# Kernel tuning notes

Measured on AMD Instinct MI355X. Metric: run time of the kernel, lower is better.

## Reference

```python
import jax, jax.numpy as jnp
import numpy as np

D_MODEL = 1024
N_HEADS = 16
HEAD_DIM = D_MODEL // N_HEADS
D_FF = 4096
LN_EPS = 1e-5


def setup_inputs() -> dict:
    key = jax.random.key(0)
    ks = jax.random.split(key, 13)
    s = lambda fan_in: 1.0 / np.sqrt(fan_in)
    return {
        "x": jax.random.normal(ks[0], (2, 2048, D_MODEL), dtype=jnp.float32),
        "w_qkv": jax.random.uniform(ks[1], (D_MODEL, 3 * D_MODEL), jnp.float32, -s(D_MODEL), s(D_MODEL)),
        "b_qkv": jax.random.uniform(ks[2], (3 * D_MODEL,), jnp.float32, -s(D_MODEL), s(D_MODEL)),
        "w_out": jax.random.uniform(ks[3], (D_MODEL, D_MODEL), jnp.float32, -s(D_MODEL), s(D_MODEL)),
        "b_out": jax.random.uniform(ks[4], (D_MODEL,), jnp.float32, -s(D_MODEL), s(D_MODEL)),
        "w_ff1": jax.random.uniform(ks[5], (D_MODEL, D_FF), jnp.float32, -s(D_MODEL), s(D_MODEL)),
        "b_ff1": jax.random.uniform(ks[6], (D_FF,), jnp.float32, -s(D_MODEL), s(D_MODEL)),
        "w_ff2": jax.random.uniform(ks[7], (D_FF, D_MODEL), jnp.float32, -s(D_FF), s(D_FF)),
        "b_ff2": jax.random.uniform(ks[8], (D_MODEL,), jnp.float32, -s(D_FF), s(D_FF)),
        "ln1_g": jnp.ones((D_MODEL,), jnp.float32),
        "ln1_b": jnp.zeros((D_MODEL,), jnp.float32),
        "ln2_g": jnp.ones((D_MODEL,), jnp.float32),
        "ln2_b": jnp.zeros((D_MODEL,), jnp.float32),
    }


def _layer_norm(x, g, b):
    mu = jnp.mean(x, axis=-1, keepdims=True)
    var = jnp.mean(jnp.square(x - mu), axis=-1, keepdims=True)
    return (x - mu) * jax.lax.rsqrt(var + LN_EPS) * g + b


def reference(x, w_qkv, b_qkv, w_out, b_out, w_ff1, b_ff1, w_ff2, b_ff2,
              ln1_g, ln1_b, ln2_g, ln2_b):
    B, S, D = x.shape
    scale = HEAD_DIM ** -0.5
    qkv = x @ w_qkv + b_qkv                                   # [B,S,3D]
    qkv = qkv.reshape(B, S, 3, N_HEADS, HEAD_DIM)
    q, k, v = (qkv[:, :, 0], qkv[:, :, 1], qkv[:, :, 2])      # [B,S,H,Dh]
    attn = jnp.einsum("bqhd,bkhd->bhqk", q, k) * scale        # [B,H,S,S]
    attn = jax.nn.softmax(attn, axis=-1)
    o = jnp.einsum("bhqk,bkhd->bqhd", attn, v).reshape(B, S, D)
    o = o @ w_out + b_out
    x = _layer_norm(x + o, ln1_g, ln1_b)
    # FFN: Linear -> exact GELU -> Linear (dropout = 0)
    h = jax.nn.gelu(x @ w_ff1 + b_ff1, approximate=False)
    ff = h @ w_ff2 + b_ff2
    x = _layer_norm(x + ff, ln2_g, ln2_b)
    return x
```

## Files before the change

kernel.cpp:

```cpp
#include <hip/hip_runtime.h>
#include <hip/hip_bf16.h>
#include <cstdint>
#include <cstddef>

using bf16 = __hip_bfloat16;
typedef __attribute__((ext_vector_type(8))) short bf16x8;
typedef __attribute__((ext_vector_type(4))) float f32x4;

#define TOKENS 4096
#define DMODEL 1024
#define DFF    4096
#define SEQ    2048
#define NHEAD  16
#define HDIM   64
#define KVBLK  64
#define NT     (SEQ / KVBLK)
#define QSCALE 0.1803368801111f

__device__ __forceinline__ void async16(const void* g, void* l) {
  __builtin_amdgcn_global_load_lds(
      (const __attribute__((address_space(1))) void*)g,
      (__attribute__((address_space(3))) void*)l, 16, 0, 0);
}

__device__ __forceinline__ f32x4 mfma16(bf16x8 a, bf16x8 b, f32x4 c) {
  return __builtin_amdgcn_mfma_f32_16x16x32_bf16(a, b, c, 0, 0, 0);
}

__device__ __forceinline__ float exp2_fast(float x) {
  float r;
  asm("v_exp_f32 %0, %1" : "=v"(r) : "v"(x));
  return r;
}

__device__ __forceinline__ float gelu_fast(float x) {
  const float z = fabsf(x) * 0.70710678118f;
  const float t = __builtin_amdgcn_rcpf(1.f + 0.3275911f * z);
  float p = 1.061405429f;
  p = p * t - 1.453152027f;
  p = p * t + 1.421413741f;
  p = p * t - 0.284496736f;
  p = p * t + 0.254829592f;
  const float e = exp2_fast(-z * z * 1.44269504089f);
  float erf = 1.f - p * t * e;
  erf = (x < 0.f) ? -erf : erf;
  return 0.5f * x * (1.f + erf);
}

__global__ void cast_bf16_k(const float* __restrict__ src, bf16* __restrict__ dst, int n) {
  int i = (blockIdx.x * blockDim.x + threadIdx.x) * 4;
  if (i >= n) return;
  float4 v = *(const float4*)(src + i);
  dst[i + 0] = __float2bfloat16(v.x);
  dst[i + 1] = __float2bfloat16(v.y);
  dst[i + 2] = __float2bfloat16(v.z);
  dst[i + 3] = __float2bfloat16(v.w);
}

__global__ void transpose_cast_k(const float* __restrict__ src, bf16* __restrict__ dst,
                                 int K, int N) {
  __shared__ float tile[32][33];
  int nt = blockIdx.x * 32, kt = blockIdx.y * 32;
  int tx = threadIdx.x, ty = threadIdx.y;
  #pragma unroll
  for (int i = 0; i < 32; i += 8)
    tile[ty + i][tx] = src[(size_t)(kt + ty + i) * N + nt + tx];
  __syncthreads();
  #pragma unroll
  for (int i = 0; i < 32; i += 8)
    dst[(size_t)(nt + ty + i) * K + kt + tx] = __float2bfloat16(tile[tx][ty + i]);
}

template <int EPI, int BN>
__global__ __launch_bounds__(256, 2)
void gemm_bt(const bf16* __restrict__ A, const bf16* __restrict__ Bt,
             const float* __restrict__ bias, int M, int N, int K,
             float* __restrict__ outf, float* __restrict__ outf2,
             bf16* __restrict__ outb,
             bf16* __restrict__ Qb, bf16* __restrict__ Kb, bf16* __restrict__ Vtb) {
  constexpr int MR = (BN == 128) ? 4 : 2;
  __shared__ bf16 Al[2][128 * 32];
  __shared__ bf16 Bl[2][BN * 32];
  const int t = threadIdx.x;
  const int nwg = gridDim.x * gridDim.y;
  const int flat = blockIdx.y * gridDim.x + blockIdx.x;
  const int swz = (flat & 7) * (nwg >> 3) + (flat >> 3);
  const int bm = (swz / gridDim.x) * 128, bn = (swz % gridDim.x) * BN;
  const int kz = blockIdx.z;
  const int Ksub = K / gridDim.z;
  const int kb0 = kz * Ksub;
  const int wid = t >> 6, lane = t & 63, g = lane >> 4, r = lane & 15;
  const int wr = (BN == 128) ? (wid >> 1) * 64 : wid * 32;
  const int wc = (BN == 128) ? (wid & 1) * 64 : 0;

  const f32x4 zero = {0.f, 0.f, 0.f, 0.f};
  f32x4 acc[MR][4];
  #pragma unroll
  for (int i = 0; i < MR; i++)
    #pragma unroll
    for (int j = 0; j < 4; j++) acc[i][j] = zero;

  const int ar0 = t >> 2, ac = (t & 3) * 8;
  const int ar1 = ar0 + 64;
  const int ach0 = t * 16, ach1 = ach0 + 4096;

  const int NK = Ksub >> 5;
  #define STAGE(ktile, pb)                                                          \
    do {                                                                            \
      const int kk = kb0 + ((ktile) << 5);                                          \
      async16(A + (size_t)(bm + ar0) * K + kk + ac, (char*)Al[pb] + ach0);          \
      async16(A + (size_t)(bm + ar1) * K + kk + ac, (char*)Al[pb] + ach1);          \
      async16(Bt + (size_t)(bn + ar0) * K + kk + ac, (char*)Bl[pb] + ach0);         \
      if constexpr (BN == 128)                                                      \
        async16(Bt + (size_t)(bn + ar1) * K + kk + ac, (char*)Bl[pb] + ach1);       \
    } while (0)

  STAGE(0, 0);
  asm volatile("s_waitcnt vmcnt(0)" ::: "memory");
  __builtin_amdgcn_s_barrier();

  #pragma unroll 1
  for (int it = 0; it < NK; ++it) {
    const int cur = it & 1;
    if (it + 1 < NK) STAGE(it + 1, cur ^ 1);
    bf16x8 af[MR], bfr[4];
    #pragma unroll
    for (int mt = 0; mt < MR; mt++)
      af[mt] = *(const bf16x8*)&Al[cur][(wr + mt * 16 + r) * 32 + 8 * g];
    #pragma unroll
    for (int nt = 0; nt < 4; nt++)
      bfr[nt] = *(const bf16x8*)&Bl[cur][(wc + nt * 16 + r) * 32 + 8 * g];
    #pragma unroll
    for (int mt = 0; mt < MR; mt++)
      #pragma unroll
      for (int nt = 0; nt < 4; nt++)
        acc[mt][nt] = mfma16(af[mt], bfr[nt], acc[mt][nt]);
    __builtin_amdgcn_sched_barrier(0);
    asm volatile("s_waitcnt vmcnt(0)" ::: "memory");
    __builtin_amdgcn_s_barrier();
  }
  #undef STAGE

  float* __restrict__ pdst = kz ? outf2 : outf;
  #pragma unroll
  for (int nt = 0; nt < 4; nt++) {
    const int col = bn + wc + nt * 16 + r;
    const float bv = (EPI == 3) ? 0.f : bias[col];
    #pragma unroll
    for (int mt = 0; mt < MR; mt++) {
      #pragma unroll
      for (int j = 0; j < 4; j++) {
        const int row = bm + wr + mt * 16 + 4 * g + j;
        float v = acc[mt][nt][j] + bv;
        if constexpr (EPI == 0) {
          const int part = col >> 10, hd = col & 1023, h = hd >> 6, d = hd & 63;
          const int b_ = row >> 11, s_ = row & 2047;
          if (part == 0) {
            Qb[((size_t)(b_ * NHEAD + h) * SEQ + s_) * HDIM + d] =
                __float2bfloat16(v * QSCALE);
          } else if (part == 1) {
            Kb[((size_t)(b_ * NHEAD + h) * SEQ + s_) * HDIM + d] = __float2bfloat16(v);
          } else {
            Vtb[((size_t)(b_ * NHEAD + h) * HDIM + d) * SEQ + s_] = __float2bfloat16(v);
          }
        } else if constexpr (EPI == 3) {
          pdst[(size_t)row * N + col] = v;
        } else {
          outb[(size_t)row * N + col] = __float2bfloat16(gelu_fast(v));
        }
      }
    }
  }
}

__global__ __launch_bounds__(256, 4)
void attn_k(const bf16* __restrict__ Q, const bf16* __restrict__ Km,
            const bf16* __restrict__ Vt, bf16* __restrict__ O) {
  __shared__ bf16 Kl[2][KVBLK * 64];
  __shared__ bf16 Vl[2][KVBLK * 64];
  __shared__ bf16 P[4][16 * 64];
  const int b = blockIdx.x;
  const int bswz = (b & 7) * 128 + (b >> 3);
  const int bh = bswz >> 5, qb = bswz & 31;
  const int t = threadIdx.x, wid = t >> 6, lane = t & 63, g = lane >> 4, r = lane & 15;
  const int q0 = qb * 64 + wid * 16;
  const bf16* Qp = Q + (size_t)bh * SEQ * HDIM;
  const char* Kc = (const char*)(Km + (size_t)bh * SEQ * HDIM);
  const char* Vc = (const char*)(Vt + (size_t)bh * HDIM * SEQ);

  const bf16x8 qf0 = *(const bf16x8*)&Qp[(q0 + r) * HDIM + 8 * g];
  const bf16x8 qf1 = *(const bf16x8*)&Qp[(q0 + r) * HDIM + 8 * g + 32];

  const int o0 = wid * 2048 + lane * 16, o1 = o0 + 1024;
  const int cs0 = ((((o0 >> 4) & 7) ^ ((o0 >> 7) & 7)) << 4);
  const int cs1 = ((((o1 >> 4) & 7) ^ ((o1 >> 7) & 7)) << 4);
  const int kso0 = (o0 & ~127) + cs0, kso1 = (o1 & ~127) + cs1;
  const int vso0 = (o0 >> 7) * (SEQ * 2) + cs0, vso1 = (o1 >> 7) * (SEQ * 2) + cs1;

  const f32x4 zero = {0.f, 0.f, 0.f, 0.f};
  f32x4 oacc[4];
  #pragma unroll
  for (int i = 0; i < 4; i++) oacc[i] = zero;
  float mrow = -1e30f, lrow = 0.f;
  bf16* pl = P[wid];
  const int cA = ((g ^ (r & 7)) << 3), cB = (((g + 4) ^ (r & 7)) << 3);

  {
    char* kd = (char*)Kl[0]; char* vd = (char*)Vl[0];
    async16(Kc + kso0, kd + o0); async16(Kc + kso1, kd + o1);
    async16(Vc + vso0, vd + o0); async16(Vc + vso1, vd + o1);
  }

  #pragma unroll 1
  for (int tt = 0; tt < NT; ++tt) {
    if (tt + 1 < NT) {
      const char* ks = Kc + (tt + 1) * (KVBLK * HDIM * 2);
      const char* vs = Vc + (tt + 1) * (KVBLK * 2);
      char* kd = (char*)Kl[(tt + 1) & 1]; char* vd = (char*)Vl[(tt + 1) & 1];
      async16(ks + kso0, kd + o0); async16(ks + kso1, kd + o1);
      async16(vs + vso0, vd + o0); async16(vs + vso1, vd + o1);
      asm volatile("s_waitcnt vmcnt(4)" ::: "memory");
    } else {
      asm volatile("s_waitcnt vmcnt(0)" ::: "memory");
    }
    __builtin_amdgcn_sched_barrier(0);
    __builtin_amdgcn_s_barrier();
    __builtin_amdgcn_sched_barrier(0);

    const bf16* kbuf = Kl[tt & 1];
    const bf16* vbuf = Vl[tt & 1];

    f32x4 sacc[4];
    #pragma unroll
    for (int kt = 0; kt < 4; kt++) {
      const bf16* krow = kbuf + (kt * 16 + r) * 64;
      bf16x8 ka = *(const bf16x8*)&krow[cA];
      bf16x8 kb = *(const bf16x8*)&krow[cB];
      f32x4 s = zero;
      s = mfma16(ka, qf0, s);
      s = mfma16(kb, qf1, s);
      sacc[kt] = s;
    }

    float m0 = fmaxf(fmaxf(sacc[0][0], sacc[0][1]), fmaxf(sacc[0][2], sacc[0][3]));
    float m1 = fmaxf(fmaxf(sacc[1][0], sacc[1][1]), fmaxf(sacc[1][2], sacc[1][3]));
    float m2 = fmaxf(fmaxf(sacc[2][0], sacc[2][1]), fmaxf(sacc[2][2], sacc[2][3]));
    float m3 = fmaxf(fmaxf(sacc[3][0], sacc[3][1]), fmaxf(sacc[3][2], sacc[3][3]));
    float mx = fmaxf(fmaxf(m0, m1), fmaxf(m2, m3));
    mx = fmaxf(mx, __shfl_xor(mx, 16));
    mx = fmaxf(mx, __shfl_xor(mx, 32));
    const bool grow = !__all(mx <= mrow + 8.f);
    float corr = 1.f;
    if (grow) {
      const float mn = fmaxf(mrow, mx);
      corr = exp2_fast(mrow - mn);
      mrow = mn;
    }
    float sum = 0.f;
    float sv[4][4];
    #pragma unroll
    for (int kt = 0; kt < 4; kt++)
      #pragma unroll
      for (int j = 0; j < 4; j++) {
        const float p = exp2_fast(sacc[kt][j] - mrow);
        sv[kt][j] = p;
        sum += p;
      }
    sum += __shfl_xor(sum, 16);
    sum += __shfl_xor(sum, 32);
    lrow = lrow * corr + sum;

    #pragma unroll
    for (int kt = 0; kt < 4; kt++) {
      bf16 pk[4] = {__float2bfloat16(sv[kt][0]), __float2bfloat16(sv[kt][1]),
                    __float2bfloat16(sv[kt][2]), __float2bfloat16(sv[kt][3])};
      const int pc = (((kt * 2 + (g >> 1)) ^ (r & 7)) << 4) + ((g & 1) << 3);
      *(short4*)((char*)pl + r * 128 + pc) = *(const short4*)pk;
    }
    asm volatile("s_waitcnt lgkmcnt(0)" ::: "memory");
    __builtin_amdgcn_sched_barrier(0);
    const bf16x8 pf0 = *(const bf16x8*)((const char*)pl + r * 128 + (cA << 1));
    const bf16x8 pf1 = *(const bf16x8*)((const char*)pl + r * 128 + (cB << 1));

    if (grow) {
      float cq[4];
      #pragma unroll
      for (int j = 0; j < 4; j++) cq[j] = __shfl(corr, 4 * g + j);
      #pragma unroll
      for (int dt = 0; dt < 4; dt++)
        #pragma unroll
        for (int j = 0; j < 4; j++) oacc[dt][j] *= cq[j];
    }

    #pragma unroll
    for (int dt = 0; dt < 4; dt++) {
      const bf16* vrow = vbuf + (dt * 16 + r) * 64;
      bf16x8 v0 = *(const bf16x8*)&vrow[cA];
      bf16x8 v1 = *(const bf16x8*)&vrow[cB];
      oacc[dt] = mfma16(pf0, v0, oacc[dt]);
      oacc[dt] = mfma16(pf1, v1, oacc[dt]);
    }
    __builtin_amdgcn_sched_barrier(0);
    __builtin_amdgcn_s_barrier();
  }

  float lq[4];
  #pragma unroll
  for (int j = 0; j < 4; j++) lq[j] = __shfl(lrow, 4 * g + j);
  const int b_ = bh >> 4, h = bh & 15;
  #pragma unroll
  for (int dt = 0; dt < 4; dt++)
    #pragma unroll
    for (int j = 0; j < 4; j++) {
      const int tok = b_ * SEQ + q0 + 4 * g + j;
      O[(size_t)tok * DMODEL + h * HDIM + dt * 16 + r] =
          __float2bfloat16(oacc[dt][j] / lq[j]);
    }
}

__global__ __launch_bounds__(256)
void ln_fused_k(const float* __restrict__ p0, const float* __restrict__ p1,
                const float* __restrict__ bias2, const float* __restrict__ resid,
                const float* __restrict__ gw, const float* __restrict__ bw,
                float* __restrict__ outf, bf16* __restrict__ outb) {
  const int row = blockIdx.x, t = threadIdx.x;
  const size_t base = (size_t)row * DMODEL + t * 4;
  const float4 a = *(const float4*)(p0 + base);
  const float4 b = *(const float4*)(p1 + base);
  const float4 rr = *(const float4*)(resid + base);
  const float4 bb = *(const float4*)(bias2 + t * 4);
  float4 v;
  v.x = a.x + b.x + rr.x + bb.x;
  v.y = a.y + b.y + rr.y + bb.y;
  v.z = a.z + b.z + rr.z + bb.z;
  v.w = a.w + b.w + rr.w + bb.w;
  float s = v.x + v.y + v.z + v.w;
  float s2 = v.x * v.x + v.y * v.y + v.z * v.z + v.w * v.w;
  #pragma unroll
  for (int m = 1; m < 64; m <<= 1) { s += __shfl_xor(s, m); s2 += __shfl_xor(s2, m); }
  __shared__ float red[8];
  const int wid = t >> 6, lane = t & 63;
  if (lane == 0) { red[wid] = s; red[4 + wid] = s2; }
  __syncthreads();
  s = red[0] + red[1] + red[2] + red[3];
  s2 = red[4] + red[5] + red[6] + red[7];
  const float mu = s * (1.f / DMODEL);
  const float rstd = rsqrtf(s2 * (1.f / DMODEL) - mu * mu + 1e-5f);
  const float4 gv = *(const float4*)(gw + t * 4);
  const float4 bv = *(const float4*)(bw + t * 4);
  float o0 = (v.x - mu) * rstd * gv.x + bv.x;
  float o1 = (v.y - mu) * rstd * gv.y + bv.y;
  float o2 = (v.z - mu) * rstd * gv.z + bv.z;
  float o3 = (v.w - mu) * rstd * gv.w + bv.w;
  if (outf) {
    float4 ov = {o0, o1, o2, o3};
    *(float4*)(outf + base) = ov;
  }
  if (outb) {
    bf16* p = outb + base;
    p[0] = __float2bfloat16(o0); p[1] = __float2bfloat16(o1);
    p[2] = __float2bfloat16(o2); p[3] = __float2bfloat16(o3);
  }
}

extern "C" void kernel_launch(void* const* d_in, const int* in_sizes, int n_in,
                              void* d_out, int out_size, void* d_ws, size_t ws_size,
                              hipStream_t stream) {
  const float* x     = (const float*)d_in[0];
  const float* w_qkv = (const float*)d_in[1];
  const float* b_qkv = (const float*)d_in[2];
  const float* w_out = (const float*)d_in[3];
  const float* b_out = (const float*)d_in[4];
  const float* w_ff1 = (const float*)d_in[5];
  const float* b_ff1 = (const float*)d_in[6];
  const float* w_ff2 = (const float*)d_in[7];
  const float* b_ff2 = (const float*)d_in[8];
  const float* ln1_g = (const float*)d_in[9];
  const float* ln1_b = (const float*)d_in[10];
  const float* ln2_g = (const float*)d_in[11];
  const float* ln2_b = (const float*)d_in[12];
  float* out = (float*)d_out;

  char* base = (char*)d_ws;
  bf16* wqkvT = (bf16*)(base);
  bf16* woutT = (bf16*)(base + 6291456);
  bf16* wff1T = (bf16*)(base + 8388608);
  bf16* wff2T = (bf16*)(base + 16777216);
  bf16* Qb    = (bf16*)(base + 25165824);
  bf16* Kb    = (bf16*)(base + 33554432);
  bf16* Vtb   = (bf16*)(base + 41943040);
  bf16* xob   = (bf16*)(base + 50331648);
  bf16* hb    = (bf16*)(base + 25165824);
  float* pA0  = (float*)(base + 25165824);
  float* pA1  = (float*)(base + 58720256);
  float* pB0  = (float*)(base + 58720256);
  float* pB1  = (float*)(base);
  float* x1f  = (float*)(base + 75497472);
  bf16* x1b   = (bf16*)(base + 92274688);
  (void)in_sizes; (void)n_in; (void)out_size; (void)ws_size;

  dim3 tb(32, 8);
  transpose_cast_k<<<dim3(3072 / 32, 1024 / 32), tb, 0, stream>>>(w_qkv, wqkvT, 1024, 3072);
  transpose_cast_k<<<dim3(1024 / 32, 1024 / 32), tb, 0, stream>>>(w_out, woutT, 1024, 1024);
  transpose_cast_k<<<dim3(4096 / 32, 1024 / 32), tb, 0, stream>>>(w_ff1, wff1T, 1024, 4096);
  transpose_cast_k<<<dim3(1024 / 32, 4096 / 32), tb, 0, stream>>>(w_ff2, wff2T, 4096, 1024);
  cast_bf16_k<<<(TOKENS * DMODEL / 4 + 255) / 256, 256, 0, stream>>>(x, xob, TOKENS * DMODEL);

  gemm_bt<0, 128><<<dim3(3072 / 128, TOKENS / 128), 256, 0, stream>>>(
      xob, wqkvT, b_qkv, TOKENS, 3072, 1024, nullptr, nullptr, nullptr, Qb, Kb, Vtb);
  attn_k<<<dim3(1024), 256, 0, stream>>>(Qb, Kb, Vtb, xob);
  gemm_bt<3, 64><<<dim3(1024 / 64, TOKENS / 128, 2), 256, 0, stream>>>(
      xob, woutT, b_out, TOKENS, 1024, 1024, pA0, pA1, nullptr, nullptr, nullptr, nullptr);
  ln_fused_k<<<TOKENS, 256, 0, stream>>>(pA0, pA1, b_out, x, ln1_g, ln1_b, x1f, x1b);
  gemm_bt<2, 128><<<dim3(4096 / 128, TOKENS / 128), 256, 0, stream>>>(
      x1b, wff1T, b_ff1, TOKENS, 4096, 1024, nullptr, nullptr, hb, nullptr, nullptr, nullptr);
  gemm_bt<3, 64><<<dim3(1024 / 64, TOKENS / 128, 2), 256, 0, stream>>>(
      hb, wff2T, b_ff2, TOKENS, 1024, 4096, pB0, pB1, nullptr, nullptr, nullptr, nullptr);
  ln_fused_k<<<TOKENS, 256, 0, stream>>>(pB0, pB1, b_ff2, x1f, ln2_g, ln2_b, out, nullptr);
}
```

Baseline: 270.2 us.

## Process two 16-row query tiles per wave in attention to reuse K/V loads

Each wave now handles 32 query rows (two 16-row sub-tiles) instead of 16, so every block covers 128 queries and the grid halves to 512 blocks. K and V tiles read from LDS feed twice as many MFMAs, which halves K/V global traffic and LDS reads per query. The cost is more registers (launch bounds drop to 3 waves per SIMD), a larger P buffer in LDS, and fewer blocks to cover the CUs.

Measured after the change: 267.0 us. Within noise of the previous version (-1.2%).

```diff
diff --git a/kernel.cpp b/kernel.cpp
--- a/kernel.cpp
+++ b/kernel.cpp
@@ -173,23 +173,27 @@
   }
 }
 
-__global__ __launch_bounds__(256, 4)
+__global__ __launch_bounds__(256, 3)
 void attn_k(const bf16* __restrict__ Q, const bf16* __restrict__ Km,
             const bf16* __restrict__ Vt, bf16* __restrict__ O) {
   __shared__ bf16 Kl[2][KVBLK * 64];
   __shared__ bf16 Vl[2][KVBLK * 64];
-  __shared__ bf16 P[4][16 * 64];
+  __shared__ bf16 P[4][32 * 64];
   const int b = blockIdx.x;
-  const int bswz = (b & 7) * 128 + (b >> 3);
-  const int bh = bswz >> 5, qb = bswz & 31;
+  const int bswz = (b & 7) * 64 + (b >> 3);
+  const int bh = bswz >> 4, qb = bswz & 15;
   const int t = threadIdx.x, wid = t >> 6, lane = t & 63, g = lane >> 4, r = lane & 15;
-  const int q0 = qb * 64 + wid * 16;
+  const int q0 = qb * 128 + wid * 32;
   const bf16* Qp = Q + (size_t)bh * SEQ * HDIM;
   const char* Kc = (const char*)(Km + (size_t)bh * SEQ * HDIM);
   const char* Vc = (const char*)(Vt + (size_t)bh * HDIM * SEQ);
 
-  const bf16x8 qf0 = *(const bf16x8*)&Qp[(q0 + r) * HDIM + 8 * g];
-  const bf16x8 qf1 = *(const bf16x8*)&Qp[(q0 + r) * HDIM + 8 * g + 32];
+  bf16x8 qf[2][2];
+  #pragma unroll
+  for (int s = 0; s < 2; s++) {
+    qf[s][0] = *(const bf16x8*)&Qp[(q0 + 16 * s + r) * HDIM + 8 * g];
+    qf[s][1] = *(const bf16x8*)&Qp[(q0 + 16 * s + r) * HDIM + 8 * g + 32];
+  }
 
   const int o0 = wid * 2048 + lane * 16, o1 = o0 + 1024;
   const int cs0 = ((((o0 >> 4) & 7) ^ ((o0 >> 7) & 7)) << 4);
@@ -198,10 +202,12 @@
   const int vso0 = (o0 >> 7) * (SEQ * 2) + cs0, vso1 = (o1 >> 7) * (SEQ * 2) + cs1;
 
   const f32x4 zero = {0.f, 0.f, 0.f, 0.f};
-  f32x4 oacc[4];
-  #pragma unroll
-  for (int i = 0; i < 4; i++) oacc[i] = zero;
-  float mrow = -1e30f, lrow = 0.f;
+  f32x4 oacc[2][4];
+  #pragma unroll
+  for (int s = 0; s < 2; s++)
+    #pragma unroll
+    for (int i = 0; i < 4; i++) oacc[s][i] = zero;
+  float mrow[2] = {-1e30f, -1e30f}, lrow[2] = {0.f, 0.f};
   bf16* pl = P[wid];
   const int cA = ((g ^ (r & 7)) << 3), cB = (((g + 4) ^ (r & 7)) << 3);
 
@@ -230,66 +236,75 @@
     const bf16* kbuf = Kl[tt & 1];
     const bf16* vbuf = Vl[tt & 1];
 
-    f32x4 sacc[4];
+    f32x4 sacc[2][4];
     #pragma unroll
     for (int kt = 0; kt < 4; kt++) {
       const bf16* krow = kbuf + (kt * 16 + r) * 64;
       bf16x8 ka = *(const bf16x8*)&krow[cA];
       bf16x8 kb = *(const bf16x8*)&krow[cB];
-      f32x4 s = zero;
-      s = mfma16(ka, qf0, s);
-      s = mfma16(kb, qf1, s);
-      sacc[kt] = s;
-    }
-
-    float m0 = fmaxf(fmaxf(sacc[0][0], sacc[0][1]), fmaxf(sacc[0][2], sacc[0][3]));
-    float m1 = fmaxf(fmaxf(sacc[1][0], sacc[1][1]), fmaxf(sacc[1][2], sacc[1][3]));
-    float m2 = fmaxf(fmaxf(sacc[2][0], sacc[2][1]), fmaxf(sacc[2][2], sacc[2][3]));
-    float m3 = fmaxf(fmaxf(sacc[3][0], sacc[3][1]), fmaxf(sacc[3][2], sacc[3][3]));
-    float mx = fmaxf(fmaxf(m0, m1), fmaxf(m2, m3));
-    mx = fmaxf(mx, __shfl_xor(mx, 16));
-    mx = fmaxf(mx, __shfl_xor(mx, 32));
-    const bool grow = !__all(mx <= mrow + 8.f);
-    float corr = 1.f;
-    if (grow) {
-      const float mn = fmaxf(mrow, mx);
-      corr = exp2_fast(mrow - mn);
-      mrow = mn;
-    }
-    float sum = 0.f;
-    float sv[4][4];
-    #pragma unroll
-    for (int kt = 0; kt < 4; kt++)
-      #pragma unroll
-      for (int j = 0; j < 4; j++) {
-        const float p = exp2_fast(sacc[kt][j] - mrow);
-        sv[kt][j] = p;
-        sum += p;
-      }
-    sum += __shfl_xor(sum, 16);
-    sum += __shfl_xor(sum, 32);
-    lrow = lrow * corr + sum;
-
-    #pragma unroll
-    for (int kt = 0; kt < 4; kt++) {
-      bf16 pk[4] = {__float2bfloat16(sv[kt][0]), __float2bfloat16(sv[kt][1]),
-                    __float2bfloat16(sv[kt][2]), __float2bfloat16(sv[kt][3])};
-      const int pc = (((kt * 2 + (g >> 1)) ^ (r & 7)) << 4) + ((g & 1) << 3);
-      *(short4*)((char*)pl + r * 128 + pc) = *(const short4*)pk;
-    }
+      #pragma unroll
+      for (int s = 0; s < 2; s++) {
+        f32x4 sc = mfma16(ka, qf[s][0], zero);
+        sacc[s][kt] = mfma16(kb, qf[s][1], sc);
+      }
+    }
+
+    bool grow[2];
+    float corr[2];
+    #pragma unroll
+    for (int s = 0; s < 2; s++) {
+      float m0 = fmaxf(fmaxf(sacc[s][0][0], sacc[s][0][1]), fmaxf(sacc[s][0][2], sacc[s][0][3]));
+      float m1 = fmaxf(fmaxf(sacc[s][1][0], sacc[s][1][1]), fmaxf(sacc[s][1][2], sacc[s][1][3]));
+      float m2 = fmaxf(fmaxf(sacc[s][2][0], sacc[s][2][1]), fmaxf(sacc[s][2][2], sacc[s][2][3]));
+      float m3 = fmaxf(fmaxf(sacc[s][3][0], sacc[s][3][1]), fmaxf(sacc[s][3][2], sacc[s][3][3]));
+      float mx = fmaxf(fmaxf(m0, m1), fmaxf(m2, m3));
+      mx = fmaxf(mx, __shfl_xor(mx, 16));
+      mx = fmaxf(mx, __shfl_xor(mx, 32));
+      grow[s] = !__all(mx <= mrow[s] + 8.f);
+      corr[s] = 1.f;
+      if (grow[s]) {
+        const float mn = fmaxf(mrow[s], mx);
+        corr[s] = exp2_fast(mrow[s] - mn);
+        mrow[s] = mn;
+      }
+      float sum = 0.f;
+      #pragma unroll
+      for (int kt = 0; kt < 4; kt++) {
+        bf16 pk[4];
+        #pragma unroll
+        for (int j = 0; j < 4; j++) {
+          const float p = exp2_fast(sacc[s][kt][j] - mrow[s]);
+          pk[j] = __float2bfloat16(p);
+          sum += p;
+        }
+        const int pc = (((kt * 2 + (g >> 1)) ^ (r & 7)) << 4) + ((g & 1) << 3);
+        *(short4*)((char*)pl + (16 * s + r) * 128 + pc) = *(const short4*)pk;
+      }
+      sum += __shfl_xor(sum, 16);
+      sum += __shfl_xor(sum, 32);
+      lrow[s] = lrow[s] * corr[s] + sum;
+    }
+
     asm volatile("s_waitcnt lgkmcnt(0)" ::: "memory");
     __builtin_amdgcn_sched_barrier(0);
-    const bf16x8 pf0 = *(const bf16x8*)((const char*)pl + r * 128 + (cA << 1));
-    const bf16x8 pf1 = *(const bf16x8*)((const char*)pl + r * 128 + (cB << 1));
-
-    if (grow) {
-      float cq[4];
-      #pragma unroll
-      for (int j = 0; j < 4; j++) cq[j] = __shfl(corr, 4 * g + j);
-      #pragma unroll
-      for (int dt = 0; dt < 4; dt++)
+    bf16x8 pf[2][2];
+    #pragma unroll
+    for (int s = 0; s < 2; s++) {
+      pf[s][0] = *(const bf16x8*)((const char*)pl + (16 * s + r) * 128 + (cA << 1));
+      pf[s][1] = *(const bf16x8*)((const char*)pl + (16 * s + r) * 128 + (cB << 1));
+    }
+
+    #pragma unroll
+    for (int s = 0; s < 2; s++) {
+      if (grow[s]) {
+        float cq[4];
         #pragma unroll
-        for (int j = 0; j < 4; j++) oacc[dt][j] *= cq[j];
+        for (int j = 0; j < 4; j++) cq[j] = __shfl(corr[s], 4 * g + j);
+        #pragma unroll
+        for (int dt = 0; dt < 4; dt++)
+          #pragma unroll
+          for (int j = 0; j < 4; j++) oacc[s][dt][j] *= cq[j];
+      }
     }
 
     #pragma unroll
@@ -297,25 +312,31 @@
       const bf16* vrow = vbuf + (dt * 16 + r) * 64;
       bf16x8 v0 = *(const bf16x8*)&vrow[cA];
       bf16x8 v1 = *(const bf16x8*)&vrow[cB];
-      oacc[dt] = mfma16(pf0, v0, oacc[dt]);
-      oacc[dt] = mfma16(pf1, v1, oacc[dt]);
+      #pragma unroll
+      for (int s = 0; s < 2; s++) {
+        oacc[s][dt] = mfma16(pf[s][0], v0, oacc[s][dt]);
+        oacc[s][dt] = mfma16(pf[s][1], v1, oacc[s][dt]);
+      }
     }
     __builtin_amdgcn_sched_barrier(0);
     __builtin_amdgcn_s_barrier();
   }
 
-  float lq[4];
-  #pragma unroll
-  for (int j = 0; j < 4; j++) lq[j] = __shfl(lrow, 4 * g + j);
   const int b_ = bh >> 4, h = bh & 15;
   #pragma unroll
-  for (int dt = 0; dt < 4; dt++)
-    #pragma unroll
-    for (int j = 0; j < 4; j++) {
-      const int tok = b_ * SEQ + q0 + 4 * g + j;
-      O[(size_t)tok * DMODEL + h * HDIM + dt * 16 + r] =
-          __float2bfloat16(oacc[dt][j] / lq[j]);
-    }
+  for (int s = 0; s < 2; s++) {
+    float lq[4];
+    #pragma unroll
+    for (int j = 0; j < 4; j++) lq[j] = __shfl(lrow[s], 4 * g + j);
+    #pragma unroll
+    for (int dt = 0; dt < 4; dt++)
+      #pragma unroll
+      for (int j = 0; j < 4; j++) {
+        const int tok = b_ * SEQ + q0 + 16 * s + 4 * g + j;
+        O[(size_t)tok * DMODEL + h * HDIM + dt * 16 + r] =
+            __float2bfloat16(oacc[s][dt][j] / lq[j]);
+      }
+  }
 }
 
 __global__ __launch_bounds__(256)
@@ -408,7 +429,7 @@
 
   gemm_bt<0, 128><<<dim3(3072 / 128, TOKENS / 128), 256, 0, stream>>>(
       xob, wqkvT, b_qkv, TOKENS, 3072, 1024, nullptr, nullptr, nullptr, Qb, Kb, Vtb);
-  attn_k<<<dim3(1024), 256, 0, stream>>>(Qb, Kb, Vtb, xob);
+  attn_k<<<dim3(512), 256, 0, stream>>>(Qb, Kb, Vtb, xob);
   gemm_bt<3, 64><<<dim3(1024 / 64, TOKENS / 128, 2), 256, 0, stream>>>(
       xob, woutT, b_out, TOKENS, 1024, 1024, pA0, pA1, nullptr, nullptr, nullptr, nullptr);
   ln_fused_k<<<TOKENS, 256, 0, stream>>>(pA0, pA1, b_out, x, ln1_g, ln1_b, x1f, x1b);
```
